# Kernel tuning notes

Hardware: AMD Instinct MI355X
Metric: run time of the kernel (lower is better)

The kernel has to match this reference:

```python
import jax, jax.numpy as jnp
import numpy as np

D_MODEL, D_STATE, D_CONV, EXPAND = 1024, 16, 4, 2
D_INNER = EXPAND * D_MODEL          # 2048
DT_RANK = D_MODEL // 16             # 64
B, L = 2, 1024


def setup_inputs() -> dict:
    key = jax.random.key(0)
    ks = jax.random.split(key, 10)
    x = jax.random.normal(ks[0], (B, L, D_MODEL), dtype=jnp.float32)
    ln_w = jnp.ones((D_MODEL,), jnp.float32)
    ln_b = jnp.zeros((D_MODEL,), jnp.float32)
    in_proj_w = jax.random.normal(ks[1], (2 * D_INNER, D_MODEL), jnp.float32) * (D_MODEL ** -0.5)
    conv_w = jax.random.normal(ks[2], (D_INNER, 1, D_CONV), jnp.float32) * (D_CONV ** -0.5)
    conv_b = jnp.zeros((D_INNER,), jnp.float32)
    x_proj_w = jax.random.normal(ks[3], (DT_RANK + 2 * D_STATE, D_INNER), jnp.float32) * (D_INNER ** -0.5)
    dt_proj_w = jax.random.normal(ks[4], (D_INNER, DT_RANK), jnp.float32) * (DT_RANK ** -0.5)
    # dt bias: inverse-softplus of dt sampled log-uniform in [1e-3, 1e-1] (mamba init)
    dt = jnp.exp(jax.random.uniform(ks[5], (D_INNER,)) * (np.log(0.1) - np.log(1e-3)) + np.log(1e-3))
    dt_proj_b = dt + jnp.log(-jnp.expm1(-dt))
    # A_log: log of [1..d_state] repeated per channel (S4D-real init)
    A_log = jnp.log(jnp.broadcast_to(jnp.arange(1, D_STATE + 1, dtype=jnp.float32), (D_INNER, D_STATE)))
    D = jnp.ones((D_INNER,), jnp.float32)
    out_proj_w = jax.random.normal(ks[6], (D_MODEL, D_INNER), jnp.float32) * (D_INNER ** -0.5)
    return dict(x=x, ln_w=ln_w, ln_b=ln_b, in_proj_w=in_proj_w, conv_w=conv_w,
                conv_b=conv_b, x_proj_w=x_proj_w, dt_proj_w=dt_proj_w,
                dt_proj_b=dt_proj_b, A_log=A_log, D=D, out_proj_w=out_proj_w)


def _layernorm(x, w, b, eps=1e-5):
    mu = jnp.mean(x, axis=-1, keepdims=True)
    var = jnp.mean(jnp.square(x - mu), axis=-1, keepdims=True)
    return (x - mu) * jax.lax.rsqrt(var + eps) * w + b


def _mamba(h, in_proj_w, conv_w, conv_b, x_proj_w, dt_proj_w, dt_proj_b, A_log, D, out_proj_w):
    # h: (B, L, d_model)
    xz = jnp.einsum('bld,ed->ble', h, in_proj_w)          # (B,L,2*d_inner)
    x_in, z = jnp.split(xz, 2, axis=-1)                   # each (B,L,d_inner)
    # depthwise causal conv1d
    kernel = jnp.transpose(conv_w, (2, 1, 0))             # (d_conv, 1, d_inner) LIO
    x_conv = jax.lax.conv_general_dilated(
        x_in, kernel, window_strides=(1,), padding=[(D_CONV - 1, 0)],
        dimension_numbers=('NLC', 'LIO', 'NLC'), feature_group_count=D_INNER)
    x_conv = jax.nn.silu(x_conv + conv_b)                 # (B,L,d_inner)
    # input-dependent SSM parameters
    x_dbl = jnp.einsum('bld,ed->ble', x_conv, x_proj_w)   # (B,L,dt_rank+2*d_state)
    dt, B_ssm, C_ssm = jnp.split(x_dbl, [DT_RANK, DT_RANK + D_STATE], axis=-1)
    dt = jax.nn.softplus(jnp.einsum('blr,dr->bld', dt, dt_proj_w) + dt_proj_b)  # (B,L,d_inner)
    A = -jnp.exp(A_log)                                   # (d_inner, d_state)
    deltaA = jnp.exp(dt[..., None] * A)                   # (B,L,d_inner,d_state)
    deltaBu = dt[..., None] * B_ssm[:, :, None, :] * x_conv[..., None]
    # selective scan: h_t = deltaA_t * h_{t-1} + deltaBu_t (parallel associative scan over L)
    def combine(left, right):
        a_l, b_l = left
        a_r, b_r = right
        return a_l * a_r, b_l * a_r + b_r
    _, states = jax.lax.associative_scan(combine, (deltaA, deltaBu), axis=1)
    y = jnp.einsum('blds,bls->bld', states, C_ssm) + x_conv * D
    y = y * jax.nn.silu(z)
    return jnp.einsum('bld,ed->ble', y, out_proj_w)       # (B,L,d_model)


def reference(x, ln_w, ln_b, in_proj_w, conv_w, conv_b, x_proj_w, dt_proj_w,
              dt_proj_b, A_log, D, out_proj_w):
    h = _layernorm(x, ln_w, ln_b)
    return x + _mamba(h, in_proj_w, conv_w, conv_b, x_proj_w, dt_proj_w,
                      dt_proj_b, A_log, D, out_proj_w)
```

## Files before the change

kernel.cpp:

```cpp
#include <hip/hip_runtime.h>
#include <hip/hip_bf16.h>
#include <math.h>

#define DM   1024
#define DI   2048
#define DS   16
#define DTR  64
#define NB   2
#define LL   1024
#define MR   (NB*LL)
#define XDBL 96
#define NC   16
#define CL   64

typedef _Float16 half8  __attribute__((ext_vector_type(8)));
typedef _Float16 half4v __attribute__((ext_vector_type(4)));
typedef float    floatx4 __attribute__((ext_vector_type(4)));

__device__ __forceinline__ void gload_lds16(const void* g, void* l) {
  __builtin_amdgcn_global_load_lds(
      (const __attribute__((address_space(1))) void*)g,
      (__attribute__((address_space(3))) void*)l, 16, 0, 0);
}

__global__ __launch_bounds__(256) void front_kernel(
    const float* __restrict__ x, const float* __restrict__ ln_w,
    const float* __restrict__ ln_b,
    const float* __restrict__ w_in, const float* __restrict__ w_out,
    const float* __restrict__ w_xp, const float* __restrict__ w_dt,
    _Float16* __restrict__ h_h, float* __restrict__ out,
    _Float16* __restrict__ w_in_h, _Float16* __restrict__ w_out_h,
    _Float16* __restrict__ w_xp_h, _Float16* __restrict__ w_dt_h) {
  const int blk = blockIdx.x;
  if (blk < MR) {
    __shared__ float sA[4], sB[4];
    const float* xr = x + (size_t)blk * DM;
    float s = 0.f, ss = 0.f;
    for (int i = threadIdx.x; i < DM; i += 256) {
      float v = xr[i];
      s += v; ss += v * v;
    }
    for (int o = 32; o > 0; o >>= 1) {
      s  += __shfl_down(s, o, 64);
      ss += __shfl_down(ss, o, 64);
    }
    const int wid = threadIdx.x >> 6, lid = threadIdx.x & 63;
    if (lid == 0) { sA[wid] = s; sB[wid] = ss; }
    __syncthreads();
    if (threadIdx.x == 0) {
      float S = sA[0] + sA[1] + sA[2] + sA[3];
      float SS = sB[0] + sB[1] + sB[2] + sB[3];
      float mu = S / DM;
      sA[0] = mu;
      sB[0] = rsqrtf(SS / DM - mu * mu + 1e-5f);
    }
    __syncthreads();
    const float mu = sA[0], rs = sB[0];
    for (int i = threadIdx.x; i < DM; i += 256) {
      const float v = xr[i];
      out[(size_t)blk * DM + i] = v;
      h_h[(size_t)blk * DM + i] = (_Float16)((v - mu) * rs * ln_w[i] + ln_b[i]);
    }
    return;
  }
  int i = (blk - MR) * 256 + threadIdx.x;
  const int N0 = 1048576, N1 = 524288, N2 = 49152, N3 = 32768;
  const float* s; _Float16* d; int off;
  if (i < N0)            { s = w_in;  d = w_in_h;  off = i; }
  else if (i < N0+N1)    { s = w_out; d = w_out_h; off = i - N0; }
  else if (i < N0+N1+N2) { s = w_xp;  d = w_xp_h;  off = i - N0 - N1; }
  else if (i < N0+N1+N2+N3) { s = w_dt; d = w_dt_h; off = i - N0 - N1 - N2; }
  else return;
  float4 v = ((const float4*)s)[off];
  half4v h = {(_Float16)v.x, (_Float16)v.y, (_Float16)v.z, (_Float16)v.w};
  ((half4v*)d)[off] = h;
}

template <int EPI, int TN>
__global__ __launch_bounds__(256) void gemm_mfma(
    const _Float16* __restrict__ A,
    const _Float16* __restrict__ W,
    void* __restrict__ Cv, void* __restrict__ C2v, int ldc,
    int M, int N, int K, int kchunk) {
  constexpr int NT = (TN + 31) / 32;
  constexpr int WSLOT = TN / 16;
  constexpr int LPS = 2 + (WSLOT >= 8 ? 2 : 1);
  __shared__ alignas(16) _Float16 As[4][4096];
  __shared__ alignas(16) _Float16 Ws[4][4096];
  const int t = threadIdx.x;
  const int wave = t >> 6, lane = t & 63;
  const int m0 = blockIdx.y * 128, n0 = blockIdx.x * TN;
  const int k_beg = blockIdx.z * kchunk;
  const int nk = kchunk / 32;
  const int wm = (wave >> 1) * 64, wn = (wave & 1) * (TN / 2);
  floatx4 acc[4][NT];
#pragma unroll
  for (int i = 0; i < 4; i++)
#pragma unroll
    for (int j = 0; j < NT; j++) acc[i][j] = {0.f, 0.f, 0.f, 0.f};

  const int fr = lane & 15;
  const int kc8 = lane >> 4;
  const int kp = (kc8 ^ ((fr >> 1) & 3)) * 8;

  auto stage = [&](int buf, int k0) {
    for (int sl = wave; sl < 8; sl += 4) {
      const int idx = sl * 64 + lane;
      const int row = idx >> 2;
      const int kc = (idx & 3) ^ ((row >> 1) & 3);
      gload_lds16(A + (size_t)(m0 + row) * K + k0 + kc * 8, &As[buf][sl * 512]);
    }
    for (int sl = wave; sl < WSLOT; sl += 4) {
      const int idx = sl * 64 + lane;
      const int row = idx >> 2;
      const int kc = (idx & 3) ^ ((row >> 1) & 3);
      const int wrow = (n0 + row < N) ? row : 0;
      gload_lds16(W + (size_t)(n0 + wrow) * K + k0 + kc * 8, &Ws[buf][sl * 512]);
    }
  };

  const int npre = nk < 3 ? nk : 3;
  for (int p = 0; p < npre; p++) stage(p, k_beg + p * 32);

  for (int ki = 0; ki < nk; ki++) {
    const int rem = nk - 1 - ki;
    if (rem >= 2)
      asm volatile("s_waitcnt vmcnt(%0)" :: "n"(2 * LPS) : "memory");
    else if (rem == 1)
      asm volatile("s_waitcnt vmcnt(%0)" :: "n"(LPS) : "memory");
    else
      asm volatile("s_waitcnt vmcnt(0)" ::: "memory");
    __builtin_amdgcn_s_barrier();
    const int cur = ki & 3;
    half8 af[4], wf[NT];
#pragma unroll
    for (int i = 0; i < 4; i++)
      af[i] = *(const half8*)&As[cur][(wm + i * 16 + fr) * 32 + kp];
#pragma unroll
    for (int j = 0; j < NT; j++)
      wf[j] = *(const half8*)&Ws[cur][(wn + j * 16 + fr) * 32 + kp];
    __builtin_amdgcn_s_setprio(1);
#pragma unroll
    for (int i = 0; i < 4; i++)
#pragma unroll
      for (int j = 0; j < NT; j++)
        acc[i][j] = __builtin_amdgcn_mfma_f32_16x16x32_f16(af[i], wf[j], acc[i][j], 0, 0, 0);
    __builtin_amdgcn_s_setprio(0);
    if (ki + 3 < nk) stage((ki + 3) & 3, k_beg + (ki + 3) * 32);
  }

  const int col = lane & 15, rowq = lane >> 4;
#pragma unroll
  for (int i = 0; i < 4; i++) {
#pragma unroll
    for (int j = 0; j < NT; j++) {
      const int n = n0 + wn + j * 16 + col;
      if (n < N) {
#pragma unroll
        for (int r = 0; r < 4; r++) {
          const int m = m0 + wm + i * 16 + rowq * 4 + r;
          float v = acc[i][j][r];
          if (EPI == 0) {
            if (n < DI) ((_Float16*)Cv )[(size_t)m * DI + n]      = (_Float16)v;
            else        ((_Float16*)C2v)[(size_t)m * DI + n - DI] = (_Float16)v;
          } else if (EPI == 6) {
            atomicAdd(&((float*)Cv)[(size_t)m * ldc + n], v);
          }
        }
      }
    }
  }
}

__global__ __launch_bounds__(256) void dt_kernel(
    const float* __restrict__ xdbl, const _Float16* __restrict__ W,
    const float* __restrict__ bias, _Float16* __restrict__ dtb) {
  __shared__ alignas(16) _Float16 As[2][4096];
  __shared__ alignas(16) _Float16 Ws[2][2048];
  const int t = threadIdx.x, wave = t >> 6, lane = t & 63;
  const int m0 = blockIdx.y * 128, n0 = blockIdx.x * 64;
  for (int q = wave; q < 16; q += 4) {
    const int ss = q >> 3, sl = q & 7;
    const int idx = sl * 64 + lane;
    const int row = idx >> 2;
    const int kc = (idx & 3) ^ ((row >> 1) & 3);
    const float* src = xdbl + (size_t)(m0 + row) * XDBL + ss * 32 + kc * 8;
    float4 a = ((const float4*)src)[0];
    float4 b = ((const float4*)src)[1];
    half8 h = {(_Float16)a.x, (_Float16)a.y, (_Float16)a.z, (_Float16)a.w,
               (_Float16)b.x, (_Float16)b.y, (_Float16)b.z, (_Float16)b.w};
    *(half8*)&As[ss][sl * 512 + lane * 8] = h;
  }
  for (int q = wave; q < 8; q += 4) {
    const int ss = q >> 2, sw = q & 3;
    const int idx = sw * 64 + lane;
    const int row = idx >> 2;
    const int kc = (idx & 3) ^ ((row >> 1) & 3);
    gload_lds16(W + (size_t)(n0 + row) * DTR + ss * 32 + kc * 8,
                &Ws[ss][sw * 512]);
  }
  asm volatile("s_waitcnt vmcnt(0)" ::: "memory");
  __syncthreads();
  const int fr = lane & 15, kc8 = lane >> 4;
  const int kp = (kc8 ^ ((fr >> 1) & 3)) * 8;
  const int wm = (wave >> 1) * 64, wn = (wave & 1) * 32;
  floatx4 acc[4][2];
#pragma unroll
  for (int i = 0; i < 4; i++)
#pragma unroll
    for (int j = 0; j < 2; j++) acc[i][j] = {0.f, 0.f, 0.f, 0.f};
#pragma unroll
  for (int ss = 0; ss < 2; ss++) {
    half8 af[4], wf[2];
#pragma unroll
    for (int i = 0; i < 4; i++)
      af[i] = *(const half8*)&As[ss][(wm + i * 16 + fr) * 32 + kp];
#pragma unroll
    for (int j = 0; j < 2; j++)
      wf[j] = *(const half8*)&Ws[ss][(wn + j * 16 + fr) * 32 + kp];
#pragma unroll
    for (int i = 0; i < 4; i++)
#pragma unroll
      for (int j = 0; j < 2; j++)
        acc[i][j] = __builtin_amdgcn_mfma_f32_16x16x32_f16(af[i], wf[j], acc[i][j], 0, 0, 0);
  }
  const int col = lane & 15, rowq = lane >> 4;
#pragma unroll
  for (int i = 0; i < 4; i++) {
#pragma unroll
    for (int j = 0; j < 2; j++) {
      const int n = n0 + wn + j * 16 + col;
#pragma unroll
      for (int r = 0; r < 4; r++) {
        const int m = m0 + wm + i * 16 + rowq * 4 + r;
        float v = acc[i][j][r] + bias[n];
        v = (v > 20.f) ? v : __logf(1.f + __expf(v));
        dtb[(size_t)m * DI + n] = (_Float16)v;
      }
    }
  }
}

__global__ __launch_bounds__(256) void conv_silu_kernel(
    const _Float16* __restrict__ xin, const float* __restrict__ cw,
    const float* __restrict__ cb, _Float16* __restrict__ xc,
    float* __restrict__ xdbl) {
  const int idx = blockIdx.x * 256 + threadIdx.x;
  if (idx < MR * XDBL) xdbl[idx] = 0.f;
  const int d8 = idx & (DI / 8 - 1);
  const int ml = idx >> 8;
  const int l  = ml & (LL - 1);
  const int d0 = d8 * 8;
  half8 xr[4];
  const half8 zero = {0, 0, 0, 0, 0, 0, 0, 0};
#pragma unroll
  for (int k = 0; k < 4; k++) {
    const int lp = l - 3 + k;
    xr[k] = (lp >= 0) ? *(const half8*)&xin[(size_t)(ml - 3 + k) * DI + d0] : zero;
  }
  half8 o;
#pragma unroll
  for (int j = 0; j < 8; j++) {
    float acc = cb[d0 + j];
#pragma unroll
    for (int k = 0; k < 4; k++)
      acc += (float)xr[k][j] * cw[(d0 + j) * 4 + k];
    o[j] = (_Float16)(acc / (1.f + __expf(-acc)));
  }
  *(half8*)&xc[(size_t)ml * DI + d0] = o;
}

__device__ __forceinline__ bool load_a(const float* __restrict__ A_log, int d,
                                       float* a) {
  const float4* Ap = (const float4*)(A_log + (size_t)d * DS);
  bool fast = true;
#pragma unroll
  for (int i = 0; i < 4; i++) {
    float4 v = Ap[i];
    a[4 * i + 0] = -__expf(v.x); a[4 * i + 1] = -__expf(v.y);
    a[4 * i + 2] = -__expf(v.z); a[4 * i + 3] = -__expf(v.w);
  }
#pragma unroll
  for (int s = 0; s < DS; s++)
    fast = fast && (fabsf(a[s] + (float)(s + 1)) < 1e-4f);
  return fast;
}

__global__ __launch_bounds__(256) void scan_phase1(
    const _Float16* __restrict__ xc,
    const float* __restrict__ xdbl,
    const _Float16* __restrict__ dtm,
    const float* __restrict__ A_log,
    float* __restrict__ HE,
    float* __restrict__ SA) {
  __shared__ float Bs[CL][DS];
  const int bi = blockIdx.x;
  const int dblk = bi & 7;
  const int c = (bi >> 3) & (NC - 1);
  const int b = bi >> 7;
  const int t = threadIdx.x;
  const int d = dblk * 256 + t;
  const int mlbase = b * LL + c * CL;

  for (int i = t; i < CL * DS; i += 256) {
    int tt = i >> 4, s = i & 15;
    Bs[tt][s] = xdbl[(size_t)(mlbase + tt) * XDBL + DTR + s];
  }

  float a[DS];
  const bool fast = load_a(A_log, d, a);
  float h[DS];
#pragma unroll
  for (int s = 0; s < DS; s++) h[s] = 0.f;
  float S = 0.f;
  __syncthreads();

  if (fast) {
    for (int tt = 0; tt < CL; tt++) {
      const size_t ml = mlbase + tt;
      const float dtv = (float)dtm[ml * DI + d];
      const float u   = (float)xc[ml * DI + d];
      const float du  = dtv * u;
      S += dtv;
      const float r = __expf(-dtv);
      float P = 1.f;
#pragma unroll
      for (int s = 0; s < DS; s++) {
        P *= r;
        h[s] = P * h[s] + du * Bs[tt][s];
      }
    }
  } else {
    for (int tt = 0; tt < CL; tt++) {
      const size_t ml = mlbase + tt;
      const float dtv = (float)dtm[ml * DI + d];
      const float u   = (float)xc[ml * DI + d];
      const float du  = dtv * u;
      S += dtv;
#pragma unroll
      for (int s = 0; s < DS; s++)
        h[s] = __expf(dtv * a[s]) * h[s] + du * Bs[tt][s];
    }
  }
  const size_t base = ((size_t)(b * NC + c) * DS) * DI + d;
#pragma unroll
  for (int s = 0; s < DS; s++) HE[base + (size_t)s * DI] = h[s];
  SA[(size_t)(b * NC + c) * DI + d] = S;
}

__global__ __launch_bounds__(256) void scan_phase2(
    const float* __restrict__ A_log,
    const float* __restrict__ SA,
    float* __restrict__ HE) {
  const int idx = blockIdx.x * 256 + threadIdx.x;
  const int d = idx & (DI - 1);
  const int s = (idx >> 11) & (DS - 1);
  const int b = idx >> 15;
  const float a = -__expf(A_log[(size_t)d * DS + s]);
  float Hc = 0.f;
  for (int c = 0; c < NC; c++) {
    const size_t o = ((size_t)(b * NC + c) * DS + s) * DI + d;
    const float he = HE[o];
    const float P = __expf(a * SA[(size_t)(b * NC + c) * DI + d]);
    HE[o] = Hc;
    Hc = P * Hc + he;
  }
}

__global__ __launch_bounds__(256) void scan_phase3(
    const _Float16* __restrict__ xc,
    const float* __restrict__ xdbl,
    const _Float16* __restrict__ dtm,
    const _Float16* __restrict__ zbuf,
    const float* __restrict__ A_log,
    const float* __restrict__ Dvec,
    const float* __restrict__ HE,
    _Float16* __restrict__ y) {
  __shared__ float Bs[CL][DS];
  __shared__ float Cs[CL][DS];
  const int bi = blockIdx.x;
  const int dblk = bi & 7;
  const int c = (bi >> 3) & (NC - 1);
  const int b = bi >> 7;
  const int t = threadIdx.x;
  const int d = dblk * 256 + t;
  const int mlbase = b * LL + c * CL;

  for (int i = t; i < CL * DS; i += 256) {
    int tt = i >> 4, s = i & 15;
    const size_t ro = (size_t)(mlbase + tt) * XDBL + DTR + s;
    Bs[tt][s] = xdbl[ro];
    Cs[tt][s] = xdbl[ro + DS];
  }

  float a[DS];
  const bool fast = load_a(A_log, d, a);
  float h[DS];
  const size_t base = ((size_t)(b * NC + c) * DS) * DI + d;
#pragma unroll
  for (int s = 0; s < DS; s++) h[s] = HE[base + (size_t)s * DI];
  const float Dv = Dvec[d];
  __syncthreads();

  if (fast) {
    for (int tt = 0; tt < CL; tt++) {
      const size_t ml = mlbase + tt;
      const float dtv = (float)dtm[ml * DI + d];
      const float u   = (float)xc[ml * DI + d];
      const float du  = dtv * u;
      const float r = __expf(-dtv);
      float P = 1.f, p = 0.f;
#pragma unroll
      for (int s = 0; s < DS; s++) {
        P *= r;
        h[s] = P * h[s] + du * Bs[tt][s];
        p += h[s] * Cs[tt][s];
      }
      const float zv = (float)zbuf[ml * DI + d];
      const float sil = zv / (1.f + __expf(-zv));
      y[ml * DI + d] = (_Float16)((p + u * Dv) * sil);
    }
  } else {
    for (int tt = 0; tt < CL; tt++) {
      const size_t ml = mlbase + tt;
      const float dtv = (float)dtm[ml * DI + d];
      const float u   = (float)xc[ml * DI + d];
      const float du  = dtv * u;
      float p = 0.f;
#pragma unroll
      for (int s = 0; s < DS; s++) {
        h[s] = __expf(dtv * a[s]) * h[s] + du * Bs[tt][s];
        p += h[s] * Cs[tt][s];
      }
      const float zv = (float)zbuf[ml * DI + d];
      const float sil = zv / (1.f + __expf(-zv));
      y[ml * DI + d] = (_Float16)((p + u * Dv) * sil);
    }
  }
}

extern "C" void kernel_launch(void* const* d_in, const int* in_sizes, int n_in,
                              void* d_out, int out_size, void* d_ws, size_t ws_size,
                              hipStream_t stream) {
  const float* x         = (const float*)d_in[0];
  const float* ln_w      = (const float*)d_in[1];
  const float* ln_b      = (const float*)d_in[2];
  const float* in_proj_w = (const float*)d_in[3];
  const float* conv_w    = (const float*)d_in[4];
  const float* conv_b    = (const float*)d_in[5];
  const float* x_proj_w  = (const float*)d_in[6];
  const float* dt_proj_w = (const float*)d_in[7];
  const float* dt_proj_b = (const float*)d_in[8];
  const float* A_log     = (const float*)d_in[9];
  const float* Dvec      = (const float*)d_in[10];
  const float* out_proj_w= (const float*)d_in[11];
  float* out = (float*)d_out;

  char* ws = (char*)d_ws;
  _Float16* h_h      = (_Float16*)ws;
  _Float16* xin_h    = (_Float16*)(ws + 4194304);
  _Float16* y_h      = xin_h;
  _Float16* z_h      = (_Float16*)(ws + 12582912);
  _Float16* xc_h     = (_Float16*)(ws + 20971520);
  _Float16* dtb_h    = (_Float16*)(ws + 29360128);
  float*    x_dbl    = (float*)   (ws + 46137344);
  float*    SA       = (float*)   (ws + 46923776);
  float*    HE       = (float*)   (ws + 47710208);
  _Float16* w_in_h   = (_Float16*)(ws + 56098816);
  _Float16* w_out_h  = (_Float16*)(ws + 64487424);
  _Float16* w_xp_h   = (_Float16*)(ws + 68681728);
  _Float16* w_dt_h   = (_Float16*)(ws + 69074944);

  front_kernel<<<MR + 6464, 256, 0, stream>>>(
      x, ln_w, ln_b, in_proj_w, out_proj_w, x_proj_w, dt_proj_w,
      h_h, out, w_in_h, w_out_h, w_xp_h, w_dt_h);

  gemm_mfma<0, 128><<<dim3(2 * DI / 128, MR / 128, 1), 256, 0, stream>>>(
      h_h, w_in_h, xin_h, z_h, 0, MR, 2 * DI, DM, DM);

  conv_silu_kernel<<<(MR * DI / 8) / 256, 256, 0, stream>>>(
      xin_h, conv_w, conv_b, xc_h, x_dbl);

  gemm_mfma<6, 96><<<dim3(1, MR / 128, 32), 256, 0, stream>>>(
      xc_h, w_xp_h, x_dbl, nullptr, XDBL, MR, XDBL, DI, DI / 32);

  dt_kernel<<<dim3(DI / 64, MR / 128), 256, 0, stream>>>(
      x_dbl, w_dt_h, dt_proj_b, dtb_h);

  scan_phase1<<<NB * NC * (DI / 256), 256, 0, stream>>>(
      xc_h, x_dbl, dtb_h, A_log, HE, SA);
  scan_phase2<<<(NB * DS * DI) / 256, 256, 0, stream>>>(A_log, SA, HE);
  scan_phase3<<<NB * NC * (DI / 256), 256, 0, stream>>>(
      xc_h, x_dbl, dtb_h, z_h, A_log, Dvec, HE, y_h);

  gemm_mfma<6, 128><<<dim3(DM / 128, MR / 128, 4), 256, 0, stream>>>(
      y_h, w_out_h, out, nullptr, DM, MR, DM, DI, DI / 4);
}
```

Before: 265.1 us.

## Fuse conv into x_proj, restructure scan into two passes, drop atomics

Fuses the depthwise conv+SiLU into the x_proj GEMM, which now writes fp16 split-K partials that the dt kernel and the scans reduce. This removes the atomic accumulation and the zeroing pass. The scan moves to 32-length chunks: a first pass computes local outputs, the cumulative dt and chunk states, and a final pass rebuilds the carry-in state from all previous chunks and adds its contribution. This drops the separate phase-2 kernel. The out_proj now runs without split-K and adds the residual x directly instead of copying x and using atomics, and the A tables are precomputed once. The risks are fp16 accumulation of partials and of the cumulative dt sum, which could cost accuracy, and redundant partial reads and O(NC) carry loops in the final scan pass.

```diff
diff --git a/kernel.cpp b/kernel.cpp
--- a/kernel.cpp
+++ b/kernel.cpp
@@ -10,8 +10,8 @@
 #define LL   1024
 #define MR   (NB*LL)
 #define XDBL 96
-#define NC   16
-#define CL   64
+#define NC   32
+#define CL   32
 
 typedef _Float16 half8  __attribute__((ext_vector_type(8)));
 typedef _Float16 half4v __attribute__((ext_vector_type(4)));
@@ -28,9 +28,11 @@
     const float* __restrict__ ln_b,
     const float* __restrict__ w_in, const float* __restrict__ w_out,
     const float* __restrict__ w_xp, const float* __restrict__ w_dt,
-    _Float16* __restrict__ h_h, float* __restrict__ out,
+    const float* __restrict__ A_log,
+    _Float16* __restrict__ h_h,
     _Float16* __restrict__ w_in_h, _Float16* __restrict__ w_out_h,
-    _Float16* __restrict__ w_xp_h, _Float16* __restrict__ w_dt_h) {
+    _Float16* __restrict__ w_xp_h, _Float16* __restrict__ w_dt_h,
+    float* __restrict__ atab, unsigned char* __restrict__ aflag) {
   const int blk = blockIdx.x;
   if (blk < MR) {
     __shared__ float sA[4], sB[4];
@@ -56,10 +58,22 @@
     }
     __syncthreads();
     const float mu = sA[0], rs = sB[0];
-    for (int i = threadIdx.x; i < DM; i += 256) {
-      const float v = xr[i];
-      out[(size_t)blk * DM + i] = v;
-      h_h[(size_t)blk * DM + i] = (_Float16)((v - mu) * rs * ln_w[i] + ln_b[i]);
+    for (int i = threadIdx.x; i < DM; i += 256)
+      h_h[(size_t)blk * DM + i] = (_Float16)((xr[i] - mu) * rs * ln_w[i] + ln_b[i]);
+    return;
+  }
+  if (blk >= MR + 6464) {
+    const int d = (blk - (MR + 6464)) * 256 + threadIdx.x;
+    if (d < DI) {
+      bool fast = true;
+      float a[DS];
+#pragma unroll
+      for (int s = 0; s < DS; s++) {
+        a[s] = -__expf(A_log[(size_t)d * DS + s]);
+        atab[(size_t)d * DS + s] = a[s];
+        fast = fast && (fabsf(a[s] + (float)(s + 1)) < 1e-4f);
+      }
+      aflag[d] = fast ? 1 : 0;
     }
     return;
   }
@@ -163,8 +177,9 @@
           if (EPI == 0) {
             if (n < DI) ((_Float16*)Cv )[(size_t)m * DI + n]      = (_Float16)v;
             else        ((_Float16*)C2v)[(size_t)m * DI + n - DI] = (_Float16)v;
-          } else if (EPI == 6) {
-            atomicAdd(&((float*)Cv)[(size_t)m * ldc + n], v);
+          } else if (EPI == 7) {
+            ((float*)Cv)[(size_t)m * ldc + n] =
+                ((const float*)C2v)[(size_t)m * ldc + n] + v;
           }
         }
       }
@@ -172,8 +187,90 @@
   }
 }
 
+__global__ __launch_bounds__(256) void xproj_conv(
+    const _Float16* __restrict__ xin, const _Float16* __restrict__ W,
+    const float* __restrict__ cw, const float* __restrict__ cb,
+    _Float16* __restrict__ part) {
+  __shared__ alignas(16) _Float16 As[4][4096];
+  __shared__ alignas(16) _Float16 Ws[4][3072];
+  const int t = threadIdx.x, wave = t >> 6, lane = t & 63;
+  const int m0 = blockIdx.y * 128;
+  const int k0 = blockIdx.z * 128;
+  for (int q = t; q < 2048; q += 256) {
+    const int ss = q >> 9, idx = q & 511;
+    const int row = idx >> 2;
+    const int kc = (idx & 3) ^ ((row >> 1) & 3);
+    const int m = m0 + row;
+    const int l = m & (LL - 1);
+    const int dbase = k0 + ss * 32 + kc * 8;
+    float accv[8];
+#pragma unroll
+    for (int j = 0; j < 8; j++) accv[j] = cb[dbase + j];
+#pragma unroll
+    for (int k = 0; k < 4; k++) {
+      const int lp = l - 3 + k;
+      if (lp >= 0) {
+        half8 xv = *(const half8*)&xin[(size_t)(m - 3 + k) * DI + dbase];
+#pragma unroll
+        for (int j = 0; j < 8; j++)
+          accv[j] += (float)xv[j] * cw[(dbase + j) * 4 + k];
+      }
+    }
+    half8 o;
+#pragma unroll
+    for (int j = 0; j < 8; j++)
+      o[j] = (_Float16)(accv[j] / (1.f + __expf(-accv[j])));
+    *(half8*)&As[ss][idx * 8] = o;
+  }
+  for (int q = wave; q < 24; q += 4) {
+    const int ss = q / 6, sw = q % 6;
+    const int idx = sw * 64 + lane;
+    const int row = idx >> 2;
+    const int kc = (idx & 3) ^ ((row >> 1) & 3);
+    gload_lds16(W + (size_t)row * DI + k0 + ss * 32 + kc * 8, &Ws[ss][sw * 512]);
+  }
+  asm volatile("s_waitcnt vmcnt(0)" ::: "memory");
+  __syncthreads();
+  const int fr = lane & 15, kc8 = lane >> 4;
+  const int kp = (kc8 ^ ((fr >> 1) & 3)) * 8;
+  const int wm = (wave >> 1) * 64, wn = (wave & 1) * 48;
+  floatx4 acc[4][3];
+#pragma unroll
+  for (int i = 0; i < 4; i++)
+#pragma unroll
+    for (int j = 0; j < 3; j++) acc[i][j] = {0.f, 0.f, 0.f, 0.f};
+#pragma unroll
+  for (int ss = 0; ss < 4; ss++) {
+    half8 af[4], wf[3];
+#pragma unroll
+    for (int i = 0; i < 4; i++)
+      af[i] = *(const half8*)&As[ss][(wm + i * 16 + fr) * 32 + kp];
+#pragma unroll
+    for (int j = 0; j < 3; j++)
+      wf[j] = *(const half8*)&Ws[ss][(wn + j * 16 + fr) * 32 + kp];
+#pragma unroll
+    for (int i = 0; i < 4; i++)
+#pragma unroll
+      for (int j = 0; j < 3; j++)
+        acc[i][j] = __builtin_amdgcn_mfma_f32_16x16x32_f16(af[i], wf[j], acc[i][j], 0, 0, 0);
+  }
+  const int col = lane & 15, rowq = lane >> 4;
+#pragma unroll
+  for (int i = 0; i < 4; i++) {
+#pragma unroll
+    for (int j = 0; j < 3; j++) {
+      const int n = wn + j * 16 + col;
+#pragma unroll
+      for (int r = 0; r < 4; r++) {
+        const int m = m0 + wm + i * 16 + rowq * 4 + r;
+        part[((size_t)blockIdx.z * MR + m) * XDBL + n] = (_Float16)acc[i][j][r];
+      }
+    }
+  }
+}
+
 __global__ __launch_bounds__(256) void dt_kernel(
-    const float* __restrict__ xdbl, const _Float16* __restrict__ W,
+    const _Float16* __restrict__ part, const _Float16* __restrict__ W,
     const float* __restrict__ bias, _Float16* __restrict__ dtb) {
   __shared__ alignas(16) _Float16 As[2][4096];
   __shared__ alignas(16) _Float16 Ws[2][2048];
@@ -184,12 +281,17 @@
     const int idx = sl * 64 + lane;
     const int row = idx >> 2;
     const int kc = (idx & 3) ^ ((row >> 1) & 3);
-    const float* src = xdbl + (size_t)(m0 + row) * XDBL + ss * 32 + kc * 8;
-    float4 a = ((const float4*)src)[0];
-    float4 b = ((const float4*)src)[1];
-    half8 h = {(_Float16)a.x, (_Float16)a.y, (_Float16)a.z, (_Float16)a.w,
-               (_Float16)b.x, (_Float16)b.y, (_Float16)b.z, (_Float16)b.w};
-    *(half8*)&As[ss][sl * 512 + lane * 8] = h;
+    const int cbase = ss * 32 + kc * 8;
+    float a8[8] = {0.f, 0.f, 0.f, 0.f, 0.f, 0.f, 0.f, 0.f};
+#pragma unroll
+    for (int z = 0; z < 16; z++) {
+      half8 p = *(const half8*)&part[((size_t)z * MR + m0 + row) * XDBL + cbase];
+#pragma unroll
+      for (int j = 0; j < 8; j++) a8[j] += (float)p[j];
+    }
+    half8 h = {(_Float16)a8[0], (_Float16)a8[1], (_Float16)a8[2], (_Float16)a8[3],
+               (_Float16)a8[4], (_Float16)a8[5], (_Float16)a8[6], (_Float16)a8[7]};
+    *(half8*)&As[ss][idx * 8] = h;
   }
   for (int q = wave; q < 8; q += 4) {
     const int ss = q >> 2, sw = q & 3;
@@ -241,201 +343,166 @@
   }
 }
 
-__global__ __launch_bounds__(256) void conv_silu_kernel(
-    const _Float16* __restrict__ xin, const float* __restrict__ cw,
-    const float* __restrict__ cb, _Float16* __restrict__ xc,
-    float* __restrict__ xdbl) {
-  const int idx = blockIdx.x * 256 + threadIdx.x;
-  if (idx < MR * XDBL) xdbl[idx] = 0.f;
-  const int d8 = idx & (DI / 8 - 1);
-  const int ml = idx >> 8;
-  const int l  = ml & (LL - 1);
-  const int d0 = d8 * 8;
-  half8 xr[4];
-  const half8 zero = {0, 0, 0, 0, 0, 0, 0, 0};
-#pragma unroll
-  for (int k = 0; k < 4; k++) {
-    const int lp = l - 3 + k;
-    xr[k] = (lp >= 0) ? *(const half8*)&xin[(size_t)(ml - 3 + k) * DI + d0] : zero;
-  }
-  half8 o;
-#pragma unroll
-  for (int j = 0; j < 8; j++) {
-    float acc = cb[d0 + j];
-#pragma unroll
-    for (int k = 0; k < 4; k++)
-      acc += (float)xr[k][j] * cw[(d0 + j) * 4 + k];
-    o[j] = (_Float16)(acc / (1.f + __expf(-acc)));
-  }
-  *(half8*)&xc[(size_t)ml * DI + d0] = o;
-}
-
-__device__ __forceinline__ bool load_a(const float* __restrict__ A_log, int d,
-                                       float* a) {
-  const float4* Ap = (const float4*)(A_log + (size_t)d * DS);
-  bool fast = true;
-#pragma unroll
-  for (int i = 0; i < 4; i++) {
-    float4 v = Ap[i];
-    a[4 * i + 0] = -__expf(v.x); a[4 * i + 1] = -__expf(v.y);
-    a[4 * i + 2] = -__expf(v.z); a[4 * i + 3] = -__expf(v.w);
-  }
-#pragma unroll
-  for (int s = 0; s < DS; s++)
-    fast = fast && (fabsf(a[s] + (float)(s + 1)) < 1e-4f);
-  return fast;
-}
-
-__global__ __launch_bounds__(256) void scan_phase1(
-    const _Float16* __restrict__ xc,
-    const float* __restrict__ xdbl,
-    const _Float16* __restrict__ dtm,
-    const float* __restrict__ A_log,
-    float* __restrict__ HE,
-    float* __restrict__ SA) {
-  __shared__ float Bs[CL][DS];
-  const int bi = blockIdx.x;
-  const int dblk = bi & 7;
-  const int c = (bi >> 3) & (NC - 1);
-  const int b = bi >> 7;
-  const int t = threadIdx.x;
-  const int d = dblk * 256 + t;
-  const int mlbase = b * LL + c * CL;
-
-  for (int i = t; i < CL * DS; i += 256) {
-    int tt = i >> 4, s = i & 15;
-    Bs[tt][s] = xdbl[(size_t)(mlbase + tt) * XDBL + DTR + s];
-  }
-
-  float a[DS];
-  const bool fast = load_a(A_log, d, a);
-  float h[DS];
-#pragma unroll
-  for (int s = 0; s < DS; s++) h[s] = 0.f;
-  float S = 0.f;
-  __syncthreads();
-
-  if (fast) {
-    for (int tt = 0; tt < CL; tt++) {
-      const size_t ml = mlbase + tt;
-      const float dtv = (float)dtm[ml * DI + d];
-      const float u   = (float)xc[ml * DI + d];
-      const float du  = dtv * u;
-      S += dtv;
-      const float r = __expf(-dtv);
-      float P = 1.f;
-#pragma unroll
-      for (int s = 0; s < DS; s++) {
-        P *= r;
-        h[s] = P * h[s] + du * Bs[tt][s];
-      }
-    }
-  } else {
-    for (int tt = 0; tt < CL; tt++) {
-      const size_t ml = mlbase + tt;
-      const float dtv = (float)dtm[ml * DI + d];
-      const float u   = (float)xc[ml * DI + d];
-      const float du  = dtv * u;
-      S += dtv;
-#pragma unroll
-      for (int s = 0; s < DS; s++)
-        h[s] = __expf(dtv * a[s]) * h[s] + du * Bs[tt][s];
-    }
-  }
-  const size_t base = ((size_t)(b * NC + c) * DS) * DI + d;
-#pragma unroll
-  for (int s = 0; s < DS; s++) HE[base + (size_t)s * DI] = h[s];
-  SA[(size_t)(b * NC + c) * DI + d] = S;
-}
-
-__global__ __launch_bounds__(256) void scan_phase2(
-    const float* __restrict__ A_log,
-    const float* __restrict__ SA,
-    float* __restrict__ HE) {
-  const int idx = blockIdx.x * 256 + threadIdx.x;
-  const int d = idx & (DI - 1);
-  const int s = (idx >> 11) & (DS - 1);
-  const int b = idx >> 15;
-  const float a = -__expf(A_log[(size_t)d * DS + s]);
-  float Hc = 0.f;
-  for (int c = 0; c < NC; c++) {
-    const size_t o = ((size_t)(b * NC + c) * DS + s) * DI + d;
-    const float he = HE[o];
-    const float P = __expf(a * SA[(size_t)(b * NC + c) * DI + d]);
-    HE[o] = Hc;
-    Hc = P * Hc + he;
-  }
-}
-
-__global__ __launch_bounds__(256) void scan_phase3(
-    const _Float16* __restrict__ xc,
-    const float* __restrict__ xdbl,
-    const _Float16* __restrict__ dtm,
-    const _Float16* __restrict__ zbuf,
-    const float* __restrict__ A_log,
+__global__ __launch_bounds__(256) void scan_p1(
+    const _Float16* __restrict__ xin, const _Float16* __restrict__ part,
+    const _Float16* dtb,
+    const float* __restrict__ atab, const unsigned char* __restrict__ aflag,
+    const float* __restrict__ cw, const float* __restrict__ cb,
     const float* __restrict__ Dvec,
-    const float* __restrict__ HE,
-    _Float16* __restrict__ y) {
+    float* __restrict__ HE, float* __restrict__ SA,
+    _Float16* __restrict__ pl, _Float16* cd) {
   __shared__ float Bs[CL][DS];
   __shared__ float Cs[CL][DS];
   const int bi = blockIdx.x;
   const int dblk = bi & 7;
   const int c = (bi >> 3) & (NC - 1);
-  const int b = bi >> 7;
+  const int b = bi >> 8;
   const int t = threadIdx.x;
   const int d = dblk * 256 + t;
   const int mlbase = b * LL + c * CL;
 
   for (int i = t; i < CL * DS; i += 256) {
-    int tt = i >> 4, s = i & 15;
-    const size_t ro = (size_t)(mlbase + tt) * XDBL + DTR + s;
-    Bs[tt][s] = xdbl[ro];
-    Cs[tt][s] = xdbl[ro + DS];
-  }
-
+    const int tt = i >> 4, s = i & 15;
+    float sb = 0.f, sc = 0.f;
+#pragma unroll
+    for (int z = 0; z < 16; z++) {
+      const size_t ro = ((size_t)z * MR + mlbase + tt) * XDBL;
+      sb += (float)part[ro + DTR + s];
+      sc += (float)part[ro + DTR + DS + s];
+    }
+    Bs[tt][s] = sb;
+    Cs[tt][s] = sc;
+  }
+
+  const bool fast = aflag[d] != 0;
   float a[DS];
-  const bool fast = load_a(A_log, d, a);
+  if (!fast) {
+#pragma unroll
+    for (int s = 0; s < DS; s++) a[s] = atab[(size_t)d * DS + s];
+  }
+  float cw4[4];
+#pragma unroll
+  for (int k = 0; k < 4; k++) cw4[k] = cw[d * 4 + k];
+  const float cbv = cb[d], Dv = Dvec[d];
+  float w0 = 0.f, w1 = 0.f, w2 = 0.f;
+  if (c > 0) {
+    w0 = (float)xin[(size_t)(mlbase - 3) * DI + d];
+    w1 = (float)xin[(size_t)(mlbase - 2) * DI + d];
+    w2 = (float)xin[(size_t)(mlbase - 1) * DI + d];
+  }
   float h[DS];
-  const size_t base = ((size_t)(b * NC + c) * DS) * DI + d;
-#pragma unroll
-  for (int s = 0; s < DS; s++) h[s] = HE[base + (size_t)s * DI];
-  const float Dv = Dvec[d];
+#pragma unroll
+  for (int s = 0; s < DS; s++) h[s] = 0.f;
+  float S = 0.f;
   __syncthreads();
 
-  if (fast) {
-    for (int tt = 0; tt < CL; tt++) {
-      const size_t ml = mlbase + tt;
-      const float dtv = (float)dtm[ml * DI + d];
-      const float u   = (float)xc[ml * DI + d];
-      const float du  = dtv * u;
+  for (int tt = 0; tt < CL; tt++) {
+    const size_t ml = mlbase + tt;
+    const float xv = (float)xin[ml * DI + d];
+    float u = cbv + w0 * cw4[0] + w1 * cw4[1] + w2 * cw4[2] + xv * cw4[3];
+    u = u / (1.f + __expf(-u));
+    w0 = w1; w1 = w2; w2 = xv;
+    const float dtv = (float)dtb[ml * DI + d];
+    const float du = dtv * u;
+    S += dtv;
+    float p = 0.f;
+    if (fast) {
       const float r = __expf(-dtv);
-      float P = 1.f, p = 0.f;
+      float P = 1.f;
 #pragma unroll
       for (int s = 0; s < DS; s++) {
         P *= r;
         h[s] = P * h[s] + du * Bs[tt][s];
         p += h[s] * Cs[tt][s];
       }
-      const float zv = (float)zbuf[ml * DI + d];
-      const float sil = zv / (1.f + __expf(-zv));
-      y[ml * DI + d] = (_Float16)((p + u * Dv) * sil);
-    }
-  } else {
-    for (int tt = 0; tt < CL; tt++) {
-      const size_t ml = mlbase + tt;
-      const float dtv = (float)dtm[ml * DI + d];
-      const float u   = (float)xc[ml * DI + d];
-      const float du  = dtv * u;
-      float p = 0.f;
+    } else {
 #pragma unroll
       for (int s = 0; s < DS; s++) {
         h[s] = __expf(dtv * a[s]) * h[s] + du * Bs[tt][s];
         p += h[s] * Cs[tt][s];
       }
-      const float zv = (float)zbuf[ml * DI + d];
-      const float sil = zv / (1.f + __expf(-zv));
-      y[ml * DI + d] = (_Float16)((p + u * Dv) * sil);
-    }
+    }
+    pl[ml * DI + d] = (_Float16)(p + u * Dv);
+    cd[ml * DI + d] = (_Float16)S;
+  }
+  const size_t base = ((size_t)(b * NC + c) * DS) * DI + d;
+#pragma unroll
+  for (int s = 0; s < DS; s++) HE[base + (size_t)s * DI] = h[s];
+  SA[(size_t)(b * NC + c) * DI + d] = S;
+}
+
+__global__ __launch_bounds__(256) void scan_fin(
+    const _Float16* __restrict__ part, const _Float16* __restrict__ pl,
+    const _Float16* __restrict__ cd, const _Float16* __restrict__ zbuf,
+    const float* __restrict__ HE, const float* __restrict__ SA,
+    const float* __restrict__ atab, const unsigned char* __restrict__ aflag,
+    _Float16* __restrict__ y) {
+  __shared__ float Cs[CL][DS];
+  const int bi = blockIdx.x;
+  const int dseg = bi & 7;
+  const int c = (bi >> 3) & (NC - 1);
+  const int b = bi >> 8;
+  const int t = threadIdx.x;
+  const int d = dseg * 256 + t;
+  const int mlbase = b * LL + c * CL;
+
+  for (int i = t; i < CL * DS; i += 256) {
+    const int tt = i >> 4, s = i & 15;
+    float sc = 0.f;
+#pragma unroll
+    for (int z = 0; z < 16; z++)
+      sc += (float)part[((size_t)z * MR + mlbase + tt) * XDBL + DTR + DS + s];
+    Cs[tt][s] = sc;
+  }
+
+  const bool fast = aflag[d] != 0;
+  float a[DS];
+  if (!fast) {
+#pragma unroll
+    for (int s = 0; s < DS; s++) a[s] = atab[(size_t)d * DS + s];
+  }
+  float hc[DS];
+#pragma unroll
+  for (int s = 0; s < DS; s++) hc[s] = 0.f;
+  for (int cc = 0; cc < c; cc++) {
+    const float Sv = SA[(size_t)(b * NC + cc) * DI + d];
+    const size_t hbase = ((size_t)(b * NC + cc) * DS) * DI + d;
+    if (fast) {
+      const float r = __expf(-Sv);
+      float P = 1.f;
+#pragma unroll
+      for (int s = 0; s < DS; s++) {
+        P *= r;
+        hc[s] = P * hc[s] + HE[hbase + (size_t)s * DI];
+      }
+    } else {
+#pragma unroll
+      for (int s = 0; s < DS; s++)
+        hc[s] = __expf(a[s] * Sv) * hc[s] + HE[hbase + (size_t)s * DI];
+    }
+  }
+  __syncthreads();
+
+  for (int tt = 0; tt < CL; tt++) {
+    const size_t ml = mlbase + tt;
+    const float cum = (float)cd[ml * DI + d];
+    float acc = (float)pl[ml * DI + d];
+    if (fast) {
+      const float q = __expf(-cum);
+      float Q = 1.f;
+#pragma unroll
+      for (int s = 0; s < DS; s++) {
+        Q *= q;
+        acc += Q * hc[s] * Cs[tt][s];
+      }
+    } else {
+#pragma unroll
+      for (int s = 0; s < DS; s++)
+        acc += __expf(a[s] * cum) * hc[s] * Cs[tt][s];
+    }
+    const float zv = (float)zbuf[ml * DI + d];
+    const float sil = zv / (1.f + __expf(-zv));
+    y[ml * DI + d] = (_Float16)(acc * sil);
   }
 }
 
@@ -461,38 +528,39 @@
   _Float16* xin_h    = (_Float16*)(ws + 4194304);
   _Float16* y_h      = xin_h;
   _Float16* z_h      = (_Float16*)(ws + 12582912);
-  _Float16* xc_h     = (_Float16*)(ws + 20971520);
+  _Float16* pl_h     = (_Float16*)(ws + 20971520);
   _Float16* dtb_h    = (_Float16*)(ws + 29360128);
-  float*    x_dbl    = (float*)   (ws + 46137344);
+  _Float16* cd_h     = dtb_h;
   float*    SA       = (float*)   (ws + 46923776);
+  float*    atab     = (float*)   (ws + 47448064);
+  unsigned char* aflag = (unsigned char*)(ws + 47579136);
   float*    HE       = (float*)   (ws + 47710208);
   _Float16* w_in_h   = (_Float16*)(ws + 56098816);
   _Float16* w_out_h  = (_Float16*)(ws + 64487424);
   _Float16* w_xp_h   = (_Float16*)(ws + 68681728);
   _Float16* w_dt_h   = (_Float16*)(ws + 69074944);
-
-  front_kernel<<<MR + 6464, 256, 0, stream>>>(
-      x, ln_w, ln_b, in_proj_w, out_proj_w, x_proj_w, dt_proj_w,
-      h_h, out, w_in_h, w_out_h, w_xp_h, w_dt_h);
+  _Float16* xp_part  = (_Float16*)(ws + 69337088);
+
+  front_kernel<<<MR + 6464 + 8, 256, 0, stream>>>(
+      x, ln_w, ln_b, in_proj_w, out_proj_w, x_proj_w, dt_proj_w, A_log,
+      h_h, w_in_h, w_out_h, w_xp_h, w_dt_h, atab, aflag);
 
   gemm_mfma<0, 128><<<dim3(2 * DI / 128, MR / 128, 1), 256, 0, stream>>>(
       h_h, w_in_h, xin_h, z_h, 0, MR, 2 * DI, DM, DM);
 
-  conv_silu_kernel<<<(MR * DI / 8) / 256, 256, 0, stream>>>(
-      xin_h, conv_w, conv_b, xc_h, x_dbl);
-
-  gemm_mfma<6, 96><<<dim3(1, MR / 128, 32), 256, 0, stream>>>(
-      xc_h, w_xp_h, x_dbl, nullptr, XDBL, MR, XDBL, DI, DI / 32);
+  xproj_conv<<<dim3(1, MR / 128, 16), 256, 0, stream>>>(
+      xin_h, w_xp_h, conv_w, conv_b, xp_part);
 
   dt_kernel<<<dim3(DI / 64, MR / 128), 256, 0, stream>>>(
-      x_dbl, w_dt_h, dt_proj_b, dtb_h);
-
-  scan_phase1<<<NB * NC * (DI / 256), 256, 0, stream>>>(
-      xc_h, x_dbl, dtb_h, A_log, HE, SA);
-  scan_phase2<<<(NB * DS * DI) / 256, 256, 0, stream>>>(A_log, SA, HE);
-  scan_phase3<<<NB * NC * (DI / 256), 256, 0, stream>>>(
-      xc_h, x_dbl, dtb_h, z_h, A_log, Dvec, HE, y_h);
-
-  gemm_mfma<6, 128><<<dim3(DM / 128, MR / 128, 4), 256, 0, stream>>>(
-      y_h, w_out_h, out, nullptr, DM, MR, DM, DI, DI / 4);
-}
+      xp_part, w_dt_h, dt_proj_b, dtb_h);
+
+  scan_p1<<<NB * NC * (DI / 256), 256, 0, stream>>>(
+      xin_h, xp_part, dtb_h, atab, aflag, conv_w, conv_b, Dvec,
+      HE, SA, pl_h, cd_h);
+
+  scan_fin<<<NB * NC * (DI / 256), 256, 0, stream>>>(
+      xp_part, pl_h, cd_h, z_h, HE, SA, atab, aflag, y_h);
+
+  gemm_mfma<7, 128><<<dim3(DM / 128, MR / 128, 1), 256, 0, stream>>>(
+      y_h, w_out_h, out, (void*)x, DM, MR, DM, DI, DI);
+}
```

After: 303.7 us. 14.6% more time.
